# Kernel optimization log

Measured on AMD Instinct MI355X. Metric: run time of the kernel, lower is better.

The kernel has to match this reference:

```python
import jax, jax.numpy as jnp
import numpy as np

N_NODES = 50000
N_EDGES = 500000
NEG_SLOPE = 0.2  # PyG GATConv default leaky_relu slope
EPS = 1e-16


def gat_conv(x, src, dst, W, a_src, a_dst, b, heads, ch):
    """PyG-style GATConv (concat=True), self-loops assumed already in src/dst."""
    n = x.shape[0]
    h = (x @ W).reshape(n, heads, ch)                      # [N,H,C]
    alpha_s = jnp.sum(h * a_src, axis=-1)                  # [N,H]
    alpha_d = jnp.sum(h * a_dst, axis=-1)                  # [N,H]
    e = jax.nn.leaky_relu(alpha_s[src] + alpha_d[dst], NEG_SLOPE)  # [E,H]
    m = jax.ops.segment_max(e, dst, num_segments=n)        # [N,H] segment softmax (stable)
    m = jnp.where(jnp.isfinite(m), m, 0.0)
    ex = jnp.exp(e - m[dst])
    den = jax.ops.segment_sum(ex, dst, num_segments=n)
    alpha = ex / (den[dst] + EPS)                          # [E,H]
    msg = h[src] * alpha[..., None]                        # [E,H,C] gather->weight
    out = jax.ops.segment_sum(msg, dst, num_segments=n)    # [N,H,C] scatter-add
    return out.reshape(n, heads * ch) + b


def setup_inputs() -> dict:
    key = jax.random.key(0)
    ks = jax.random.split(key, 11)
    s = 0.05
    return {
        "edge_index": jax.random.randint(ks[0], (2, N_EDGES), 0, N_NODES, dtype=jnp.int32),
        "batch_size": 8,
        "node_emb": jax.random.normal(ks[1], (N_NODES, 64), jnp.float32),
        "W1": jax.random.normal(ks[2], (64, 512), jnp.float32) * s,
        "att_src1": jax.random.normal(ks[3], (4, 128), jnp.float32) * s,
        "att_dst1": jax.random.normal(ks[4], (4, 128), jnp.float32) * s,
        "b1": jax.random.normal(ks[5], (512,), jnp.float32) * s,
        "W2": jax.random.normal(ks[6], (512, 256), jnp.float32) * s,
        "att_src2": jax.random.normal(ks[7], (1, 256), jnp.float32) * s,
        "att_dst2": jax.random.normal(ks[8], (1, 256), jnp.float32) * s,
        "b2": jax.random.normal(ks[9], (256,), jnp.float32) * s,
    }


def reference(edge_index, batch_size, node_emb, W1, att_src1, att_dst1, b1,
              W2, att_src2, att_dst2, b2):
    # add self-loops (PyG GATConv default add_self_loops=True)
    loops = jnp.arange(N_NODES, dtype=edge_index.dtype)
    src = jnp.concatenate([edge_index[0], loops])
    dst = jnp.concatenate([edge_index[1], loops])
    x = gat_conv(node_emb, src, dst, W1, att_src1, att_dst1, b1, heads=4, ch=128)
    x = jax.nn.elu(x)  # dropout inactive at eval
    x = gat_conv(x, src, dst, W2, att_src2, att_dst2, b2, heads=1, ch=256)
    g = jnp.mean(x, axis=0, keepdims=True)                 # [1, 256]
    return jnp.broadcast_to(g, (batch_size, g.shape[1]))
```

## Files before the change

### kernel.cpp

```cpp
#include <hip/hip_runtime.h>
#include <cstdint>

#define N_NODES 50000
#define N_EDGES 500000
#define ET (N_NODES + N_EDGES)
#define WSB 256
#define EBLK 2149
#define NEBLK 12500

typedef unsigned short u16;
typedef unsigned int   u32;
typedef __attribute__((ext_vector_type(8))) short short8;
typedef __attribute__((ext_vector_type(4))) float f32x4;

__device__ __forceinline__ float bf2f(u16 s) { return __uint_as_float((u32)s << 16); }
__device__ __forceinline__ u16 f2bf(float f) {
  u32 u = __float_as_uint(f);
  u32 r = (u + 0x7FFFu + ((u >> 16) & 1u)) >> 16;
  return (u16)r;
}
__device__ __forceinline__ void unpack8(uint4 u, float* f) {
  f[0] = __uint_as_float(u.x << 16); f[1] = __uint_as_float(u.x & 0xffff0000u);
  f[2] = __uint_as_float(u.y << 16); f[3] = __uint_as_float(u.y & 0xffff0000u);
  f[4] = __uint_as_float(u.z << 16); f[5] = __uint_as_float(u.z & 0xffff0000u);
  f[6] = __uint_as_float(u.w << 16); f[7] = __uint_as_float(u.w & 0xffff0000u);
}
__device__ __forceinline__ float lrelu(float v) { return v >= 0.f ? v : 0.2f * v; }

__device__ __forceinline__ int detect_fp32(const u16* __restrict__ ne) {
  int lane = threadIdx.x & 63;
  int bad = 0;
  #pragma unroll
  for (int j = 0; j < 2; ++j) {
    float v = fabsf(bf2f(ne[lane * 2 + j * 128]));
    bad += (!(v < 16.0f)) ? 1 : 0;
  }
  #pragma unroll
  for (int off = 32; off >= 1; off >>= 1) bad += __shfl_xor(bad, off, 64);
  return bad > 16;
}

__global__ __launch_bounds__(256) void k_prep(const int* __restrict__ ei,
                                              int* __restrict__ deg,
                                              const void* __restrict__ ne_src,
                                              u16* __restrict__ ne_b,
                                              const void* __restrict__ w1src,
                                              u16* __restrict__ W1t,
                                              const void* __restrict__ w2src,
                                              u16* __restrict__ W2t,
                                              const void* s0, const void* s1,
                                              const void* s2, const void* s3,
                                              const void* s4, const void* s5,
                                              float* d0, float* d1, float* d2,
                                              float* d3, float* d4, float* d5) {
  int b = blockIdx.x, tid = threadIdx.x;
  if (b < EBLK) {
    int e = b * 256 + tid;
    if (e < ET) {
      int d = (e < N_EDGES) ? ei[N_EDGES + e] : (e - N_EDGES);
      atomicAdd(&deg[d], 1);
    }
    return;
  }
  int fp32 = detect_fp32((const u16*)ne_src);
  b -= EBLK;
  if (b < NEBLK) {
    int i = b * 256 + tid;
    ne_b[i] = fp32 ? f2bf(((const float*)ne_src)[i]) : ((const u16*)ne_src)[i];
    return;
  }
  b -= NEBLK;
  if (b < 640) {
    int i = b * 256 + tid;
    if (i < 32768) {
      int n = i >> 6, k = i & 63;
      W1t[i] = fp32 ? f2bf(((const float*)w1src)[k * 512 + n])
                    : ((const u16*)w1src)[k * 512 + n];
    } else {
      int j = i - 32768;
      int n = j >> 9, k = j & 511;
      W2t[j] = fp32 ? f2bf(((const float*)w2src)[k * 256 + n])
                    : ((const u16*)w2src)[k * 256 + n];
    }
    return;
  }
  b -= 640;
  {
    int i = b * 256 + tid;
    const void* s; float* d; int j;
    if      (i < 512)  { s = s0; d = d0; j = i; }
    else if (i < 1024) { s = s1; d = d1; j = i - 512; }
    else if (i < 1536) { s = s2; d = d2; j = i - 1024; }
    else if (i < 1792) { s = s3; d = d3; j = i - 1536; }
    else if (i < 2048) { s = s4; d = d4; j = i - 1792; }
    else if (i < 2304) { s = s5; d = d5; j = i - 2048; }
    else return;
    d[j] = fp32 ? ((const float*)s)[j] : bf2f(((const u16*)s)[j]);
  }
}

__global__ void k_vab(const u16* __restrict__ W1t,
                      const float* __restrict__ as1v, const float* __restrict__ ad1v,
                      float* __restrict__ va_s, float* __restrict__ va_d,
                      const u16* __restrict__ W2t,
                      const float* __restrict__ as2v, const float* __restrict__ ad2v,
                      float* __restrict__ va2_s, float* __restrict__ va2_d) {
  if (blockIdx.x == 0) {
    int t = threadIdx.x;
    int h = t >> 6, k = t & 63;
    float s = 0.f, d = 0.f;
    for (int c = 0; c < 128; ++c) {
      float w = bf2f(W1t[(size_t)(h * 128 + c) * 64 + k]);
      s = fmaf(as1v[h * 128 + c], w, s);
      d = fmaf(ad1v[h * 128 + c], w, d);
    }
    va_s[t] = s;
    va_d[t] = d;
  } else {
    int k = (blockIdx.x - 1) * 256 + threadIdx.x;
    if (k >= 512) return;
    float s = 0.f, d = 0.f;
    for (int c = 0; c < 256; ++c) {
      float w = bf2f(W2t[(size_t)c * 512 + k]);
      s = fmaf(as2v[c], w, s);
      d = fmaf(ad2v[c], w, d);
    }
    va2_s[k] = s;
    va2_d[k] = d;
  }
}

__global__ __launch_bounds__(1024) void k_partial(const int* __restrict__ deg,
                                                  int* __restrict__ excl,
                                                  int* __restrict__ btot) {
  __shared__ int wsum[16];
  int tid = threadIdx.x;
  int i = blockIdx.x * 1024 + tid;
  int v = (i < N_NODES) ? deg[i] : 0;
  int lane = tid & 63, wid = tid >> 6;
  int incl = v;
  #pragma unroll
  for (int off = 1; off < 64; off <<= 1) {
    int t = __shfl_up(incl, off, 64);
    if (lane >= off) incl += t;
  }
  if (lane == 63) wsum[wid] = incl;
  __syncthreads();
  int prefix = 0;
  for (int w = 0; w < wid; ++w) prefix += wsum[w];
  if (i < N_NODES) excl[i] = prefix + incl - v;
  if (tid == 1023) btot[blockIdx.x] = prefix + incl;
}

__global__ void k_bases(const int* __restrict__ btot, int* __restrict__ bbase,
                        int* __restrict__ row_off, int nb) {
  int lane = threadIdx.x;
  int v = (lane < nb) ? btot[lane] : 0;
  int incl = v;
  #pragma unroll
  for (int off = 1; off < 64; off <<= 1) {
    int t = __shfl_up(incl, off, 64);
    if (lane >= off) incl += t;
  }
  if (lane < nb) bbase[lane] = incl - v;
  if (lane == 0) row_off[N_NODES] = ET;
}

__global__ __launch_bounds__(1024) void k_add(int* __restrict__ row_off,
                                              int* __restrict__ cursor,
                                              const int* __restrict__ bbase) {
  int i = blockIdx.x * 1024 + threadIdx.x;
  if (i < N_NODES) {
    int r = row_off[i] + bbase[blockIdx.x];
    row_off[i] = r;
    cursor[i] = r;
  }
}

__global__ __launch_bounds__(256) void k_scal(const int* __restrict__ ei,
                                              int* __restrict__ cursor,
                                              int* __restrict__ srcs,
                                              const u16* __restrict__ ne_b,
                                              const float* __restrict__ va_s,
                                              const float* __restrict__ va_d,
                                              float* __restrict__ as_o,
                                              float* __restrict__ ad_o) {
  int b = blockIdx.x;
  if (b < EBLK) {
    int e = b * 256 + threadIdx.x;
    if (e >= ET) return;
    int s, d;
    if (e < N_EDGES) { s = ei[e]; d = ei[N_EDGES + e]; }
    else { s = d = e - N_EDGES; }
    int pos = atomicAdd(&cursor[d], 1);
    srcs[pos] = s;
    return;
  }
  b -= EBLK;
  int wid = threadIdx.x >> 6, lane = threadIdx.x & 63;
  int n = b * 4 + wid;
  if (n >= N_NODES) return;
  int h = lane >> 4, il = lane & 15;
  u32 u2[2];
  *(uint2*)u2 = *(const uint2*)(ne_b + (size_t)n * 64 + il * 4);
  float f[4];
  f[0] = bf2f((u16)u2[0]); f[1] = bf2f((u16)(u2[0] >> 16));
  f[2] = bf2f((u16)u2[1]); f[3] = bf2f((u16)(u2[1] >> 16));
  float4 vs = *(const float4*)(va_s + h * 64 + il * 4);
  float4 vd = *(const float4*)(va_d + h * 64 + il * 4);
  float s = f[0] * vs.x + f[1] * vs.y + f[2] * vs.z + f[3] * vs.w;
  float d = f[0] * vd.x + f[1] * vd.y + f[2] * vd.z + f[3] * vd.w;
  #pragma unroll
  for (int off = 8; off >= 1; off >>= 1) {
    s += __shfl_xor(s, off, 64);
    d += __shfl_xor(d, off, 64);
  }
  if (il == 0) { as_o[n * 4 + h] = s; ad_o[n * 4 + h] = d; }
}

#define LSTR 40
__global__ __launch_bounds__(256) void k_gemm_l1(const u16* __restrict__ aggne,
                                                 const u16* __restrict__ W1t,
                                                 const float* __restrict__ b1f,
                                                 const float* __restrict__ va2_s,
                                                 const float* __restrict__ va2_d,
                                                 u16* __restrict__ x2,
                                                 float* __restrict__ as2,
                                                 float* __restrict__ ad2, int M) {
  __shared__ __align__(16) u16 As[128 * LSTR];
  __shared__ __align__(16) u16 Bs[128 * LSTR];
  const int tid = threadIdx.x;
  const int lane = tid & 63, wid = tid >> 6;
  const int wr = (wid >> 1) * 64, wc = (wid & 1) * 64;
  const int m = lane & 15, q = lane >> 4;
  const int row0 = blockIdx.x * 128, head = blockIdx.y;
  const u16* Bt = W1t + (size_t)head * 128 * 64;
  f32x4 acc[4][4] = {};
  #pragma unroll
  for (int kk = 0; kk < 64; kk += 32) {
    #pragma unroll
    for (int i = 0; i < 2; ++i) {
      int v = tid + i * 256;
      int row = v >> 2, ch = (v & 3) * 8;
      uint4 u = make_uint4(0, 0, 0, 0);
      int gr = row0 + row;
      if (gr < M) u = *(const uint4*)(aggne + (size_t)gr * 256 + head * 64 + kk + ch);
      *(uint4*)(As + row * LSTR + ch) = u;
    }
    #pragma unroll
    for (int i = 0; i < 2; ++i) {
      int v = tid + i * 256;
      int row = v >> 2, ch = (v & 3) * 8;
      uint4 u = *(const uint4*)(Bt + (size_t)row * 64 + kk + ch);
      *(uint4*)(Bs + row * LSTR + ch) = u;
    }
    __syncthreads();
    short8 af[4], bfr[4];
    #pragma unroll
    for (int t = 0; t < 4; ++t) {
      af[t]  = *(const short8*)(As + (wr + t * 16 + m) * LSTR + q * 8);
      bfr[t] = *(const short8*)(Bs + (wc + t * 16 + m) * LSTR + q * 8);
    }
    #pragma unroll
    for (int mt = 0; mt < 4; ++mt)
      #pragma unroll
      for (int nt = 0; nt < 4; ++nt)
        acc[mt][nt] = __builtin_amdgcn_mfma_f32_16x16x32_bf16(
            af[mt], bfr[nt], acc[mt][nt], 0, 0, 0);
    __syncthreads();
  }
  float vs[4], vd[4];
  #pragma unroll
  for (int nt = 0; nt < 4; ++nt) {
    int gc = head * 128 + wc + nt * 16 + m;
    vs[nt] = va2_s[gc];
    vd[nt] = va2_d[gc];
  }
  float ps[16] = {}, pd[16] = {};
  #pragma unroll
  for (int mt = 0; mt < 4; ++mt) {
    int grb = row0 + wr + mt * 16 + q * 4;
    #pragma unroll
    for (int nt = 0; nt < 4; ++nt) {
      int lc = wc + nt * 16 + m;
      float bias = b1f[head * 128 + lc];
      #pragma unroll
      for (int r = 0; r < 4; ++r) {
        int gr = grb + r;
        if (gr < M) {
          float v = acc[mt][nt][r] + bias;
          v = v > 0.f ? v : (__expf(v) - 1.0f);
          x2[(size_t)gr * 512 + head * 128 + lc] = f2bf(v);
          ps[mt * 4 + r] = fmaf(v, vs[nt], ps[mt * 4 + r]);
          pd[mt * 4 + r] = fmaf(v, vd[nt], pd[mt * 4 + r]);
        }
      }
    }
  }
  #pragma unroll
  for (int mt = 0; mt < 4; ++mt)
    #pragma unroll
    for (int r = 0; r < 4; ++r) {
      float s = ps[mt * 4 + r], d = pd[mt * 4 + r];
      #pragma unroll
      for (int off = 8; off >= 1; off >>= 1) {
        s += __shfl_xor(s, off, 64);
        d += __shfl_xor(d, off, 64);
      }
      int gr = row0 + wr + mt * 16 + q * 4 + r;
      if (m == 0 && gr < M) {
        atomicAdd(&as2[gr], s);
        atomicAdd(&ad2[gr], d);
      }
    }
}

__global__ __launch_bounds__(256) void k_fagg1(const int* __restrict__ row_off,
                                               const int* __restrict__ srcs,
                                               const u16* __restrict__ ne_b,
                                               const float* __restrict__ as1,
                                               const float* __restrict__ ad1,
                                               u16* __restrict__ aggne) {
  int wid = threadIdx.x >> 6, lane = threadIdx.x & 63;
  int n = blockIdx.x * 4 + wid;
  if (n >= N_NODES) return;
  int start = row_off[n], end = row_off[n + 1];
  int g = lane >> 4, il = lane & 15;
  float adn_g = ad1[n * 4 + g];
  float sum = 0.f;
  for (int e0 = start; e0 < end; e0 += 16) {
    int e = e0 + il;
    if (e < end) sum += __expf(lrelu(as1[srcs[e] * 4 + g] + adn_g));
  }
  #pragma unroll
  for (int off = 8; off >= 1; off >>= 1) sum += __shfl_xor(sum, off, 64);
  float inv = 1.0f / (sum + 1e-16f);
  float i_[4], d_[4];
  #pragma unroll
  for (int h = 0; h < 4; ++h) {
    i_[h] = __shfl(inv, h * 16, 64);
    d_[h] = __shfl(adn_g, h * 16, 64);
  }
  float acc[4] = {};
  for (int e0 = start; e0 < end; e0 += 64) {
    int lim = end - e0; if (lim > 64) lim = 64;
    int es = e0 + lane;
    int sreg = srcs[es < end ? es : end - 1];
    float4 a = *(const float4*)(as1 + sreg * 4);
    float wreg[4];
    wreg[0] = __expf(lrelu(a.x + d_[0])) * i_[0];
    wreg[1] = __expf(lrelu(a.y + d_[1])) * i_[1];
    wreg[2] = __expf(lrelu(a.z + d_[2])) * i_[2];
    wreg[3] = __expf(lrelu(a.w + d_[3])) * i_[3];
    int j = 0;
    for (; j + 3 < lim; j += 4) {
      int sa = __shfl(sreg, j, 64),     sb = __shfl(sreg, j + 1, 64);
      int sc = __shfl(sreg, j + 2, 64), sd = __shfl(sreg, j + 3, 64);
      float f0 = bf2f(ne_b[(size_t)sa * 64 + lane]);
      float f1 = bf2f(ne_b[(size_t)sb * 64 + lane]);
      float f2 = bf2f(ne_b[(size_t)sc * 64 + lane]);
      float f3 = bf2f(ne_b[(size_t)sd * 64 + lane]);
      #pragma unroll
      for (int h = 0; h < 4; ++h) {
        acc[h] = fmaf(__shfl(wreg[h], j, 64), f0, acc[h]);
        acc[h] = fmaf(__shfl(wreg[h], j + 1, 64), f1, acc[h]);
        acc[h] = fmaf(__shfl(wreg[h], j + 2, 64), f2, acc[h]);
        acc[h] = fmaf(__shfl(wreg[h], j + 3, 64), f3, acc[h]);
      }
    }
    for (; j < lim; ++j) {
      int sa = __shfl(sreg, j, 64);
      float f0 = bf2f(ne_b[(size_t)sa * 64 + lane]);
      #pragma unroll
      for (int h = 0; h < 4; ++h)
        acc[h] = fmaf(__shfl(wreg[h], j, 64), f0, acc[h]);
    }
  }
  #pragma unroll
  for (int h = 0; h < 4; ++h)
    aggne[(size_t)n * 256 + h * 64 + lane] = f2bf(acc[h]);
}

__global__ __launch_bounds__(256) void k_nodew(const int* __restrict__ row_off,
                                               const int* __restrict__ srcs,
                                               const float* __restrict__ as2,
                                               const float* __restrict__ ad2,
                                               float* __restrict__ c) {
  int wid = threadIdx.x >> 6, lane = threadIdx.x & 63;
  int n = blockIdx.x * 4 + wid;
  if (n >= N_NODES) return;
  int start = row_off[n], end = row_off[n + 1];
  int deg = end - start;
  float adn = ad2[n];
  if (deg <= 64) {
    int e = start + (lane < deg ? lane : 0);
    int s = srcs[e];
    float ex = (lane < deg) ? __expf(lrelu(as2[s] + adn)) : 0.f;
    float sum = ex;
    #pragma unroll
    for (int off = 32; off >= 1; off >>= 1) sum += __shfl_xor(sum, off, 64);
    float w = ex / (sum + 1e-16f);
    if (lane < deg) atomicAdd(&c[s], w);
  } else {
    float sum = 0.f;
    for (int e = start + lane; e < end; e += 64)
      sum += __expf(lrelu(as2[srcs[e]] + adn));
    #pragma unroll
    for (int off = 32; off >= 1; off >>= 1) sum += __shfl_xor(sum, off, 64);
    float inv = 1.0f / (sum + 1e-16f);
    for (int e = start + lane; e < end; e += 64) {
      int s = srcs[e];
      float w = __expf(lrelu(as2[s] + adn)) * inv;
      atomicAdd(&c[s], w);
    }
  }
}

__global__ __launch_bounds__(256) void k_wsum(const u16* __restrict__ x2,
                                              const float* __restrict__ c,
                                              float* __restrict__ s_vec) {
  __shared__ float part[4][512];
  int wid = threadIdx.x >> 6, lane = threadIdx.x & 63;
  int wglob = blockIdx.x * 4 + wid;
  float acc[8] = {};
  int n = wglob;
  for (; n + WSB * 4 < N_NODES; n += WSB * 8) {
    int n2 = n + WSB * 4;
    float c0 = c[n], c1 = c[n2];
    uint4 u0 = *(const uint4*)(x2 + (size_t)n * 512 + lane * 8);
    uint4 u1 = *(const uint4*)(x2 + (size_t)n2 * 512 + lane * 8);
    float f0[8], f1[8];
    unpack8(u0, f0); unpack8(u1, f1);
    #pragma unroll
    for (int j = 0; j < 8; ++j) {
      acc[j] = fmaf(c0, f0[j], acc[j]);
      acc[j] = fmaf(c1, f1[j], acc[j]);
    }
  }
  if (n < N_NODES) {
    float c0 = c[n];
    uint4 u0 = *(const uint4*)(x2 + (size_t)n * 512 + lane * 8);
    float f0[8];
    unpack8(u0, f0);
    #pragma unroll
    for (int j = 0; j < 8; ++j) acc[j] = fmaf(c0, f0[j], acc[j]);
  }
  #pragma unroll
  for (int j = 0; j < 8; ++j) part[wid][lane * 8 + j] = acc[j];
  __syncthreads();
  int t = threadIdx.x;
  float v0 = part[0][t] + part[1][t] + part[2][t] + part[3][t];
  float v1 = part[0][t + 256] + part[1][t + 256] + part[2][t + 256] + part[3][t + 256];
  atomicAdd(&s_vec[t], v0);
  atomicAdd(&s_vec[t + 256], v1);
}

__global__ __launch_bounds__(256) void k_tinyfinal(const float* __restrict__ s_vec,
                                                   const u16* __restrict__ W2t,
                                                   const float* __restrict__ b2f,
                                                   float* __restrict__ out,
                                                   int out_size) {
  int wid = threadIdx.x >> 6, lane = threadIdx.x & 63;
  int cbase = blockIdx.x * 64 + wid * 16;
  float sv[8];
  #pragma unroll
  for (int j = 0; j < 8; ++j) sv[j] = s_vec[lane * 8 + j];
  for (int i = 0; i < 16; ++i) {
    int cc = cbase + i;
    uint4 u = *(const uint4*)(W2t + (size_t)cc * 512 + lane * 8);
    float f[8];
    unpack8(u, f);
    float p = 0.f;
    #pragma unroll
    for (int j = 0; j < 8; ++j) p = fmaf(sv[j], f[j], p);
    #pragma unroll
    for (int off = 32; off >= 1; off >>= 1) p += __shfl_xor(p, off, 64);
    if (lane == 0) {
      float val = p * (1.0f / (float)N_NODES) + b2f[cc];
      for (int o = cc; o < out_size; o += 256) out[o] = val;
    }
  }
}

extern "C" void kernel_launch(void* const* d_in, const int* in_sizes, int n_in,
                              void* d_out, int out_size, void* d_ws, size_t ws_size,
                              hipStream_t stream) {
  (void)in_sizes; (void)n_in; (void)ws_size;
  const int* edge_index = (const int*)d_in[0];
  float* out = (float*)d_out;

  char* w = (char*)d_ws;
  size_t off = 0;
  auto alloc = [&](size_t bytes) -> void* {
    void* p = w + off;
    off += (bytes + 255) & ~(size_t)255;
    return p;
  };
  u16*   ne_b    = (u16*)  alloc((size_t)N_NODES * 64 * 2);
  u16*   W1t     = (u16*)  alloc(32768 * 2);
  u16*   W2t     = (u16*)  alloc(131072 * 2);
  float* as1v    = (float*)alloc(512 * 4);
  float* ad1v    = (float*)alloc(512 * 4);
  float* b1f     = (float*)alloc(512 * 4);
  float* as2v    = (float*)alloc(256 * 4);
  float* ad2v    = (float*)alloc(256 * 4);
  float* b2f     = (float*)alloc(256 * 4);
  float* va_s    = (float*)alloc(256 * 4);
  float* va_d    = (float*)alloc(256 * 4);
  float* va2_s   = (float*)alloc(512 * 4);
  float* va2_d   = (float*)alloc(512 * 4);
  u16*   aggne   = (u16*)  alloc((size_t)N_NODES * 256 * 2);
  u16*   x2      = (u16*)  alloc((size_t)N_NODES * 512 * 2);
  float* as1     = (float*)alloc((size_t)N_NODES * 4 * 4);
  float* ad1     = (float*)alloc((size_t)N_NODES * 4 * 4);
  size_t z0 = off;
  float* as2     = (float*)alloc((size_t)N_NODES * 4);
  float* ad2     = (float*)alloc((size_t)N_NODES * 4);
  float* cwt     = (float*)alloc((size_t)N_NODES * 4);
  float* s_vec   = (float*)alloc(512 * 4);
  int*   deg     = (int*)  alloc((size_t)N_NODES * 4);
  size_t z1 = off;
  int*   row_off = (int*)  alloc((size_t)(N_NODES + 1) * 4);
  int*   cursor  = (int*)  alloc((size_t)N_NODES * 4);
  int*   srcs    = (int*)  alloc((size_t)ET * 4);
  int*   btot    = (int*)  alloc(64 * 4);
  int*   bbase   = (int*)  alloc(64 * 4);

  hipMemsetAsync(w + z0, 0, z1 - z0, stream);

  k_prep<<<EBLK + NEBLK + 640 + 9, 256, 0, stream>>>(
      edge_index, deg, d_in[2], ne_b, d_in[3], W1t, d_in[7], W2t,
      d_in[4], d_in[5], d_in[6], d_in[8], d_in[9], d_in[10],
      as1v, ad1v, b1f, as2v, ad2v, b2f);
  k_vab<<<3, 256, 0, stream>>>(W1t, as1v, ad1v, va_s, va_d,
                               W2t, as2v, ad2v, va2_s, va2_d);

  k_partial<<<49, 1024, 0, stream>>>(deg, row_off, btot);
  k_bases  <<<1, 64, 0, stream>>>(btot, bbase, row_off, 49);
  k_add    <<<49, 1024, 0, stream>>>(row_off, cursor, bbase);

  k_scal<<<EBLK + (N_NODES + 3) / 4, 256, 0, stream>>>(
      edge_index, cursor, srcs, ne_b, va_s, va_d, as1, ad1);

  k_fagg1<<<(N_NODES + 3) / 4, 256, 0, stream>>>(row_off, srcs, ne_b, as1, ad1, aggne);
  dim3 gl1((N_NODES + 127) / 128, 4);
  k_gemm_l1<<<gl1, 256, 0, stream>>>(aggne, W1t, b1f, va2_s, va2_d, x2, as2, ad2,
                                     N_NODES);

  k_nodew<<<(N_NODES + 3) / 4, 256, 0, stream>>>(row_off, srcs, as2, ad2, cwt);
  k_wsum<<<WSB, 256, 0, stream>>>(x2, cwt, s_vec);
  k_tinyfinal<<<4, 256, 0, stream>>>(s_vec, W2t, b2f, out, out_size);
}
```

Before: 310.0 us.

## Stage GEMM epilogue through LDS and fuse softmax denominator into aggregation pass

The layer-1 GEMM epilogue now writes bf16 ELU results into padded shared memory, then each pair of threads stores a row with 16-byte vector writes and computes the attention dot products, issuing one atomic per row instead of per 16-lane group. The aggregation kernel drops the separate pass over edges that computed the softmax denominator; it accumulates unnormalized weights and the per-head sum in the same loop and divides at the end. This removes scattered 2-byte global stores, redundant edge/source gathers and extra exp work, at the cost of an extra barrier, more shared memory, and normalization applied after accumulation (slightly different rounding).

```diff
diff --git a/kernel.cpp b/kernel.cpp
--- a/kernel.cpp
+++ b/kernel.cpp
@@ -219,6 +219,7 @@
 }
 
 #define LSTR 40
+#define CPAD 136
 __global__ __launch_bounds__(256) void k_gemm_l1(const u16* __restrict__ aggne,
                                                  const u16* __restrict__ W1t,
                                                  const float* __restrict__ b1f,
@@ -227,8 +228,9 @@
                                                  u16* __restrict__ x2,
                                                  float* __restrict__ as2,
                                                  float* __restrict__ ad2, int M) {
-  __shared__ __align__(16) u16 As[128 * LSTR];
-  __shared__ __align__(16) u16 Bs[128 * LSTR];
+  __shared__ __align__(16) u16 smem[128 * CPAD];
+  u16* As = smem;
+  u16* Bs = smem + 128 * LSTR;
   const int tid = threadIdx.x;
   const int lane = tid & 63, wid = tid >> 6;
   const int wr = (wid >> 1) * 64, wc = (wid & 1) * 64;
@@ -269,50 +271,49 @@
             af[mt], bfr[nt], acc[mt][nt], 0, 0, 0);
     __syncthreads();
   }
-  float vs[4], vd[4];
-  #pragma unroll
-  for (int nt = 0; nt < 4; ++nt) {
-    int gc = head * 128 + wc + nt * 16 + m;
-    vs[nt] = va2_s[gc];
-    vd[nt] = va2_d[gc];
-  }
-  float ps[16] = {}, pd[16] = {};
+  u16* Cs = smem;
   #pragma unroll
   for (int mt = 0; mt < 4; ++mt) {
-    int grb = row0 + wr + mt * 16 + q * 4;
     #pragma unroll
     for (int nt = 0; nt < 4; ++nt) {
       int lc = wc + nt * 16 + m;
       float bias = b1f[head * 128 + lc];
       #pragma unroll
       for (int r = 0; r < 4; ++r) {
-        int gr = grb + r;
-        if (gr < M) {
-          float v = acc[mt][nt][r] + bias;
-          v = v > 0.f ? v : (__expf(v) - 1.0f);
-          x2[(size_t)gr * 512 + head * 128 + lc] = f2bf(v);
-          ps[mt * 4 + r] = fmaf(v, vs[nt], ps[mt * 4 + r]);
-          pd[mt * 4 + r] = fmaf(v, vd[nt], pd[mt * 4 + r]);
-        }
+        float v = acc[mt][nt][r] + bias;
+        v = v > 0.f ? v : (__expf(v) - 1.0f);
+        Cs[(wr + mt * 16 + q * 4 + r) * CPAD + lc] = f2bf(v);
       }
     }
   }
-  #pragma unroll
-  for (int mt = 0; mt < 4; ++mt)
-    #pragma unroll
-    for (int r = 0; r < 4; ++r) {
-      float s = ps[mt * 4 + r], d = pd[mt * 4 + r];
+  __syncthreads();
+  int row = tid >> 1, half = tid & 1;
+  int gr = row0 + row;
+  if (gr < M) {
+    const u16* src = Cs + row * CPAD + half * 64;
+    int cb = head * 128 + half * 64;
+    float s = 0.f, d = 0.f;
+    #pragma unroll
+    for (int i = 0; i < 8; ++i) {
+      uint4 u = *(const uint4*)(src + i * 8);
+      *(uint4*)(x2 + (size_t)gr * 512 + cb + i * 8) = u;
+      float f[8];
+      unpack8(u, f);
+      const float* pvs = va2_s + cb + i * 8;
+      const float* pvd = va2_d + cb + i * 8;
       #pragma unroll
-      for (int off = 8; off >= 1; off >>= 1) {
-        s += __shfl_xor(s, off, 64);
-        d += __shfl_xor(d, off, 64);
+      for (int j = 0; j < 8; ++j) {
+        s = fmaf(f[j], pvs[j], s);
+        d = fmaf(f[j], pvd[j], d);
       }
-      int gr = row0 + wr + mt * 16 + q * 4 + r;
-      if (m == 0 && gr < M) {
-        atomicAdd(&as2[gr], s);
-        atomicAdd(&ad2[gr], d);
-      }
-    }
+    }
+    s += __shfl_xor(s, 1, 64);
+    d += __shfl_xor(d, 1, 64);
+    if (half == 0) {
+      atomicAdd(&as2[gr], s);
+      atomicAdd(&ad2[gr], d);
+    }
+  }
 }
 
 __global__ __launch_bounds__(256) void k_fagg1(const int* __restrict__ row_off,
@@ -325,33 +326,23 @@
   int n = blockIdx.x * 4 + wid;
   if (n >= N_NODES) return;
   int start = row_off[n], end = row_off[n + 1];
-  int g = lane >> 4, il = lane & 15;
-  float adn_g = ad1[n * 4 + g];
-  float sum = 0.f;
-  for (int e0 = start; e0 < end; e0 += 16) {
-    int e = e0 + il;
-    if (e < end) sum += __expf(lrelu(as1[srcs[e] * 4 + g] + adn_g));
-  }
-  #pragma unroll
-  for (int off = 8; off >= 1; off >>= 1) sum += __shfl_xor(sum, off, 64);
-  float inv = 1.0f / (sum + 1e-16f);
-  float i_[4], d_[4];
-  #pragma unroll
-  for (int h = 0; h < 4; ++h) {
-    i_[h] = __shfl(inv, h * 16, 64);
-    d_[h] = __shfl(adn_g, h * 16, 64);
-  }
-  float acc[4] = {};
+  float4 adv = *(const float4*)(ad1 + n * 4);
+  float acc[4] = {}, lsum[4] = {};
   for (int e0 = start; e0 < end; e0 += 64) {
     int lim = end - e0; if (lim > 64) lim = 64;
     int es = e0 + lane;
-    int sreg = srcs[es < end ? es : end - 1];
+    int valid = es < end;
+    int sreg = srcs[valid ? es : end - 1];
     float4 a = *(const float4*)(as1 + sreg * 4);
     float wreg[4];
-    wreg[0] = __expf(lrelu(a.x + d_[0])) * i_[0];
-    wreg[1] = __expf(lrelu(a.y + d_[1])) * i_[1];
-    wreg[2] = __expf(lrelu(a.z + d_[2])) * i_[2];
-    wreg[3] = __expf(lrelu(a.w + d_[3])) * i_[3];
+    wreg[0] = __expf(lrelu(a.x + adv.x));
+    wreg[1] = __expf(lrelu(a.y + adv.y));
+    wreg[2] = __expf(lrelu(a.z + adv.z));
+    wreg[3] = __expf(lrelu(a.w + adv.w));
+    if (valid) {
+      lsum[0] += wreg[0]; lsum[1] += wreg[1];
+      lsum[2] += wreg[2]; lsum[3] += wreg[3];
+    }
     int j = 0;
     for (; j + 3 < lim; j += 4) {
       int sa = __shfl(sreg, j, 64),     sb = __shfl(sreg, j + 1, 64);
@@ -377,8 +368,16 @@
     }
   }
   #pragma unroll
+  for (int off = 32; off >= 1; off >>= 1) {
+    lsum[0] += __shfl_xor(lsum[0], off, 64);
+    lsum[1] += __shfl_xor(lsum[1], off, 64);
+    lsum[2] += __shfl_xor(lsum[2], off, 64);
+    lsum[3] += __shfl_xor(lsum[3], off, 64);
+  }
+  #pragma unroll
   for (int h = 0; h < 4; ++h)
-    aggne[(size_t)n * 256 + h * 64 + lane] = f2bf(acc[h]);
+    aggne[(size_t)n * 256 + h * 64 + lane] =
+        f2bf(acc[h] / (lsum[h] + 1e-16f));
 }
 
 __global__ __launch_bounds__(256) void k_nodew(const int* __restrict__ row_off,
```

New measurement: 311.1 us. No clear change (+0.3%).
